# Optimization experiments

Hardware: AMD Instinct MI355X
Metric: run time of the kernel (lower is better)

## Reference

```python
import jax, jax.numpy as jnp
import numpy as np

N_NODES = 50000
N_EDGES = 800000
N_GRAPHS = 512
IN_DIM, HID_DIM, EMB_DIM = 128, 256, 128
EPS = 1e-5


def setup_inputs() -> dict:
    key = jax.random.key(0)
    ks = jax.random.split(key, 12)
    x = jax.random.normal(ks[0], (N_NODES, IN_DIM), dtype=jnp.float32)
    edge_index = jax.random.randint(ks[1], (2, N_EDGES), 0, N_NODES, dtype=jnp.int32)
    batch = jnp.sort(jax.random.randint(ks[2], (N_NODES,), 0, N_GRAPHS, dtype=jnp.int32))
    s1 = 1.0 / np.sqrt(IN_DIM)
    s2 = 1.0 / np.sqrt(HID_DIM)
    return {
        "x": x,
        "edge_index": edge_index,
        "batch": batch,
        "W1": jax.random.uniform(ks[3], (IN_DIM, HID_DIM), jnp.float32, -s1, s1),
        "b1": jnp.zeros((HID_DIM,), jnp.float32),
        "gamma1": jnp.ones((HID_DIM,), jnp.float32),
        "beta1": jnp.zeros((HID_DIM,), jnp.float32),
        "W2": jax.random.uniform(ks[4], (HID_DIM, EMB_DIM), jnp.float32, -s2, s2),
        "b2": jnp.zeros((EMB_DIM,), jnp.float32),
        "gamma2": jnp.ones((EMB_DIM,), jnp.float32),
        "beta2": jnp.zeros((EMB_DIM,), jnp.float32),
    }


def _gcn_conv(x, W, b, src, dst, n_nodes):
    # PyG GCNConv: h = xW; aggregate with sym-normalized adjacency incl. self-loops; + bias
    h = x @ W  # [N, D]
    ones = jnp.ones(src.shape[0], dtype=h.dtype)
    deg = jax.ops.segment_sum(ones, dst, num_segments=n_nodes) + 1.0  # self-loop
    dinv = jax.lax.rsqrt(deg)
    norm = dinv[src] * dinv[dst]  # [E]
    msg = h[src] * norm[:, None]  # gather + scale  [E, D]
    agg = jax.ops.segment_sum(msg, dst, num_segments=n_nodes)
    agg = agg + h * (1.0 / deg)[:, None]  # self-loop contribution (norm = 1/deg)
    return agg + b


def _batchnorm(h, gamma, beta):
    mean = jnp.mean(h, axis=0)
    var = jnp.mean(jnp.square(h - mean), axis=0)  # biased, training mode
    return gamma * (h - mean) * jax.lax.rsqrt(var + EPS) + beta


def reference(x, edge_index, batch, W1, b1, gamma1, beta1, W2, b2, gamma2, beta2):
    src, dst = edge_index[0], edge_index[1]
    n = x.shape[0]
    h = _gcn_conv(x, W1, b1, src, dst, n)
    h = _batchnorm(jax.nn.relu(h), gamma1, beta1)
    h = _gcn_conv(h, W2, b2, src, dst, n)
    h = _batchnorm(jax.nn.relu(h), gamma2, beta2)
    return jax.ops.segment_max(h, batch, num_segments=N_GRAPHS)
```

## Files before the change

kernel.cpp:

```cpp
#include <hip/hip_runtime.h>
#include <math.h>

#define N_NODES 50000
#define N_EDGES 800000
#define N_GRAPHS 512
#define IN_DIM 128
#define HID_DIM 256
#define EMB_DIM 128
#define EPS 1e-5f
#define ELLW 64
#define NGROUP 8
#define GROUPN 6250
#define BLK_PER_GROUP 256
#define EPB ((N_EDGES + BLK_PER_GROUP - 1) / BLK_PER_GROUP)
#define F2B_N (N_NODES * IN_DIM / 4)
#define F2B_BLOCKS ((F2B_N + 255) / 256)
#define TW1_BLOCKS ((HID_DIM * IN_DIM + 255) / 256)
#define DINV_BLOCKS ((N_NODES + 255) / 256)

typedef __attribute__((ext_vector_type(8))) short bf16x8;
typedef __attribute__((ext_vector_type(4))) float f32x4;

static __device__ __forceinline__ unsigned short f2b(float f) {
    unsigned u = __float_as_uint(f);
    return (unsigned short)((u + 0x7fffu + ((u >> 16) & 1u)) >> 16);
}
static __device__ __forceinline__ float b2f(unsigned short h) {
    return __uint_as_float(((unsigned)h) << 16);
}

__global__ void __launch_bounds__(256) scatter_xcd(const int* __restrict__ src,
                                                   const int* __restrict__ dst,
                                                   int* __restrict__ fill,
                                                   int* __restrict__ col) {
    int b = blockIdx.x;
    int g = b & 7;
    int bs = b >> 3;
    int lo = g * GROUPN;
    int hi = lo + GROUPN;
    int e_end = min((bs + 1) * EPB, N_EDGES);
    for (int e = bs * EPB + threadIdx.x; e < e_end; e += 256) {
        int d = dst[e];
        if (d >= lo && d < hi) {
            int pos = atomicAdd(&fill[d], 1);
            pos = min(pos, ELLW - 1);
            col[(d << 6) + pos] = src[e];
        }
    }
}

__global__ void convert_kernel(const float* __restrict__ x, unsigned short* __restrict__ xbf,
                               const float* __restrict__ W1, unsigned short* __restrict__ W1t,
                               const int* __restrict__ fill, float* __restrict__ dinv) {
    int b = blockIdx.x;
    if (b < F2B_BLOCKS) {
        int i = b * 256 + threadIdx.x;
        if (i < F2B_N) {
            float4 v = ((const float4*)x)[i];
            ushort4 o;
            o.x = f2b(v.x); o.y = f2b(v.y); o.z = f2b(v.z); o.w = f2b(v.w);
            ((ushort4*)xbf)[i] = o;
        }
    } else if (b < F2B_BLOCKS + TW1_BLOCKS) {
        int j = (b - F2B_BLOCKS) * 256 + threadIdx.x;
        if (j < HID_DIM * IN_DIM) {
            int n = j >> 7;
            int k = j & 127;
            W1t[j] = f2b(W1[k * HID_DIM + n]);
        }
    } else {
        int v = (b - F2B_BLOCKS - TW1_BLOCKS) * 256 + threadIdx.x;
        if (v < N_NODES) dinv[v] = rsqrtf((float)(min(fill[v], ELLW) + 1));
    }
}

static __device__ __forceinline__ void acc8(float* acc, uint4 r, float w) {
    const unsigned* u = (const unsigned*)&r;
#pragma unroll
    for (int k = 0; k < 4; ++k) {
        float lo = __uint_as_float((u[k] & 0xFFFFu) << 16);
        float hi = __uint_as_float(u[k] & 0xFFFF0000u);
        acc[2 * k]     += w * lo;
        acc[2 * k + 1] += w * hi;
    }
}

template <bool RELU, bool OUT_BF, bool BIAS>
__global__ void __launch_bounds__(256) aggw_kernel(const unsigned short* __restrict__ h,
                                                   const float* __restrict__ dinv,
                                                   const int* __restrict__ deg,
                                                   const int* __restrict__ col,
                                                   const float* __restrict__ bias,
                                                   void* __restrict__ y) {
    int tid = threadIdx.x;
    int lane = tid & 63;
    int wid = tid >> 6;
    int v = blockIdx.x * 4 + wid;
    int g = lane >> 4;
    int p = lane & 15;

    int beg = v << 6;
    int end = beg + min(deg[v], ELLW);
    float acc[8] = {};

    for (int e = beg; e < end; e += 16) {
        int i0 = e + g, i1 = e + 4 + g, i2 = e + 8 + g, i3 = e + 12 + g;
        int c0 = min(i0, end - 1), c1 = min(i1, end - 1);
        int c2 = min(i2, end - 1), c3 = min(i3, end - 1);
        int u0 = col[c0], u1 = col[c1], u2 = col[c2], u3 = col[c3];
        float w0 = (i0 < end) ? dinv[u0] : 0.f;
        float w1 = (i1 < end) ? dinv[u1] : 0.f;
        float w2 = (i2 < end) ? dinv[u2] : 0.f;
        float w3 = (i3 < end) ? dinv[u3] : 0.f;
        uint4 d0 = *(const uint4*)(h + (size_t)u0 * 128 + p * 8);
        uint4 d1 = *(const uint4*)(h + (size_t)u1 * 128 + p * 8);
        uint4 d2 = *(const uint4*)(h + (size_t)u2 * 128 + p * 8);
        uint4 d3 = *(const uint4*)(h + (size_t)u3 * 128 + p * 8);
        acc8(acc, d0, w0);
        acc8(acc, d1, w1);
        acc8(acc, d2, w2);
        acc8(acc, d3, w3);
    }

#pragma unroll
    for (int k = 0; k < 8; ++k) {
        float a = acc[k];
        a += __shfl_xor(a, 16, 64);
        a += __shfl_xor(a, 32, 64);
        acc[k] = a;
    }

    if (g == 0) {
        uint4 selfr = *(const uint4*)(h + (size_t)v * 128 + p * 8);
        const unsigned* su = (const unsigned*)&selfr;
        float dv = dinv[v];
        float dv2 = dv * dv;
        float o[8];
#pragma unroll
        for (int k = 0; k < 4; ++k) {
            float lo = __uint_as_float((su[k] & 0xFFFFu) << 16);
            float hi = __uint_as_float(su[k] & 0xFFFF0000u);
            o[2 * k]     = dv * acc[2 * k]     + lo * dv2;
            o[2 * k + 1] = dv * acc[2 * k + 1] + hi * dv2;
        }
        if (BIAS) {
            float4 bv0 = *(const float4*)&bias[p * 8];
            float4 bv1 = *(const float4*)&bias[p * 8 + 4];
            o[0] += bv0.x; o[1] += bv0.y; o[2] += bv0.z; o[3] += bv0.w;
            o[4] += bv1.x; o[5] += bv1.y; o[6] += bv1.z; o[7] += bv1.w;
        }
        if (RELU) {
#pragma unroll
            for (int k = 0; k < 8; ++k) o[k] = fmaxf(o[k], 0.f);
        }
        if (OUT_BF) {
            uint4 packed;
            unsigned* pu = (unsigned*)&packed;
#pragma unroll
            for (int k = 0; k < 4; ++k)
                pu[k] = (unsigned)f2b(o[2 * k]) | ((unsigned)f2b(o[2 * k + 1]) << 16);
            *(uint4*)((unsigned short*)y + (size_t)v * 128 + p * 8) = packed;
        } else {
            float* yf = (float*)y + (size_t)v * 128 + p * 8;
            *(float4*)yf = make_float4(o[0], o[1], o[2], o[3]);
            *(float4*)(yf + 4) = make_float4(o[4], o[5], o[6], o[7]);
        }
    }
}

template <bool RELU>
__global__ void __launch_bounds__(256) mfma_gemm_kernel(const unsigned short* __restrict__ A,
                                                        const unsigned short* __restrict__ Bt,
                                                        const float* __restrict__ bias,
                                                        unsigned short* __restrict__ C,
                                                        int M, int N, int K) {
    const int LDT = 40;
    __shared__ unsigned short As[64 * LDT];
    __shared__ unsigned short Bs[64 * LDT];
    int tid = threadIdx.x;
    int bm = blockIdx.x * 64;
    int bn = blockIdx.y * 64;
    int lr = tid >> 2;
    int lc = (tid & 3) * 8;
    int lane = tid & 63;
    int w = tid >> 6;
    int wr = (w >> 1) * 32, wc = (w & 1) * 32;
    int l15 = lane & 15, q = lane >> 4;

    f32x4 acc[2][2] = {};
    bool arow_ok = (bm + lr) < M;
    const unsigned short* Aptr = A + (size_t)(bm + lr) * K + lc;
    const unsigned short* Bptr = Bt + (size_t)(bn + lr) * K + lc;

    for (int k0 = 0; k0 < K; k0 += 32) {
        uint4 av = arow_ok ? *(const uint4*)(Aptr + k0) : make_uint4(0u, 0u, 0u, 0u);
        uint4 bv = *(const uint4*)(Bptr + k0);
        *(uint4*)&As[lr * LDT + lc] = av;
        *(uint4*)&Bs[lr * LDT + lc] = bv;
        __syncthreads();
        bf16x8 a0 = *(const bf16x8*)&As[(wr + 0 + l15) * LDT + q * 8];
        bf16x8 a1 = *(const bf16x8*)&As[(wr + 16 + l15) * LDT + q * 8];
        bf16x8 b0 = *(const bf16x8*)&Bs[(wc + 0 + l15) * LDT + q * 8];
        bf16x8 b1 = *(const bf16x8*)&Bs[(wc + 16 + l15) * LDT + q * 8];
        acc[0][0] = __builtin_amdgcn_mfma_f32_16x16x32_bf16(a0, b0, acc[0][0], 0, 0, 0);
        acc[0][1] = __builtin_amdgcn_mfma_f32_16x16x32_bf16(a0, b1, acc[0][1], 0, 0, 0);
        acc[1][0] = __builtin_amdgcn_mfma_f32_16x16x32_bf16(a1, b0, acc[1][0], 0, 0, 0);
        acc[1][1] = __builtin_amdgcn_mfma_f32_16x16x32_bf16(a1, b1, acc[1][1], 0, 0, 0);
        __syncthreads();
    }

#pragma unroll
    for (int mi = 0; mi < 2; ++mi)
#pragma unroll
        for (int ni = 0; ni < 2; ++ni) {
            int colc = bn + wc + ni * 16 + l15;
            float bv = bias ? bias[colc] : 0.f;
#pragma unroll
            for (int r = 0; r < 4; ++r) {
                int row = bm + wr + mi * 16 + q * 4 + r;
                if (row < M) {
                    float vv = acc[mi][ni][r] + bv;
                    if (RELU) vv = fmaxf(vv, 0.f);
                    C[(size_t)row * N + colc] = f2b(vv);
                }
            }
        }
}

template <int C, bool BF>
__global__ void __launch_bounds__(256) stats_fast(const void* __restrict__ yv,
                                                  float* __restrict__ sum,
                                                  float* __restrict__ sumsq) {
    constexpr int VEC = BF ? 8 : 4;
    constexpr int NCHUNK = C / VEC;
    constexpr int ROWS = 256 / NCHUNK;
    constexpr int STRIDE = 256 * ROWS;
    __shared__ float sp[256 * VEC];
    __shared__ float qp[256 * VEC];
    int t = threadIdx.x;
    int j = t & (NCHUNK - 1);
    float s[VEC], q[VEC];
#pragma unroll
    for (int k = 0; k < VEC; ++k) { s[k] = 0.f; q[k] = 0.f; }

    const char* base = (const char*)yv + (size_t)j * 16;
    auto body = [&](int v) {
        uint4 raw = *(const uint4*)(base + (size_t)v * (C * (BF ? 2 : 4)));
        float x[VEC];
        if (BF) {
            const unsigned* u = (const unsigned*)&raw;
#pragma unroll
            for (int k = 0; k < 4; ++k) {
                x[2 * k]     = __uint_as_float((u[k] & 0xFFFFu) << 16);
                x[2 * k + 1] = __uint_as_float(u[k] & 0xFFFF0000u);
            }
        } else {
            const float* f = (const float*)&raw;
#pragma unroll
            for (int k = 0; k < VEC; ++k) x[k] = f[k];
        }
#pragma unroll
        for (int k = 0; k < VEC; ++k) { s[k] += x[k]; q[k] += x[k] * x[k]; }
    };

    int v = blockIdx.x * ROWS + (t >> 5);
    for (; v + 3 * STRIDE < N_NODES; v += 4 * STRIDE) {
        body(v); body(v + STRIDE); body(v + 2 * STRIDE); body(v + 3 * STRIDE);
    }
    for (; v < N_NODES; v += STRIDE) body(v);

#pragma unroll
    for (int k = 0; k < VEC; ++k) { sp[t * VEC + k] = s[k]; qp[t * VEC + k] = q[k]; }
    __syncthreads();
    if (t < C) {
        float ss = 0.f, qq = 0.f;
#pragma unroll
        for (int rr = 0; rr < ROWS; ++rr) {
            ss += sp[rr * (NCHUNK * VEC) + t];
            qq += qp[rr * (NCHUNK * VEC) + t];
        }
        atomicAdd(&sum[t], ss);
        atomicAdd(&sumsq[t], qq);
    }
}

__global__ void prep2_kernel(const float* __restrict__ sum1, const float* __restrict__ sumsq1,
                             const float* __restrict__ gamma1, const float* __restrict__ beta1,
                             const float* __restrict__ W2, unsigned short* __restrict__ W2pt,
                             float* __restrict__ bc2) {
    __shared__ float a1s[HID_DIM], s1s[HID_DIM];
    int t = threadIdx.x;
    {
        float m = sum1[t] * (1.f / N_NODES);
        float var = sumsq1[t] * (1.f / N_NODES) - m * m;
        float a = gamma1[t] * rsqrtf(var + EPS);
        a1s[t] = a;
        s1s[t] = beta1[t] - m * a;
    }
    __syncthreads();
    if (t < EMB_DIM) {
        float bacc = 0.f;
        for (int k = 0; k < HID_DIM; ++k) {
            float w = W2[k * EMB_DIM + t];
            W2pt[t * HID_DIM + k] = f2b(a1s[k] * w);
            bacc += s1s[k] * w;
        }
        bc2[t] = bacc;
    }
}

__global__ void __launch_bounds__(128) segmax_kernel(const float* __restrict__ y,
                                                     const float* __restrict__ sum2,
                                                     const float* __restrict__ sumsq2,
                                                     const float* __restrict__ gamma2,
                                                     const float* __restrict__ beta2,
                                                     const int* __restrict__ batch,
                                                     float* __restrict__ out) {
    __shared__ int sh[2];
    int g = blockIdx.x;
    int c = threadIdx.x;
    float mch = sum2[c] * (1.f / N_NODES);
    float var = sumsq2[c] * (1.f / N_NODES) - mch * mch;
    float ac = gamma2[c] * rsqrtf(var + EPS);
    float sc = beta2[c] - mch * ac;
    if (threadIdx.x == 0) {
        int lo = 0, hi = N_NODES;
        while (lo < hi) { int mid = (lo + hi) >> 1; if (batch[mid] < g) lo = mid + 1; else hi = mid; }
        sh[0] = lo;
        hi = N_NODES;
        while (lo < hi) { int mid = (lo + hi) >> 1; if (batch[mid] < g + 1) lo = mid + 1; else hi = mid; }
        sh[1] = lo;
    }
    __syncthreads();
    int beg = sh[0], end = sh[1];
    float m = -INFINITY;
    for (int v = beg; v < end; ++v) {
        m = fmaxf(m, fmaf(ac, y[(size_t)v * EMB_DIM + c], sc));
    }
    out[(size_t)g * EMB_DIM + c] = m;
}

extern "C" void kernel_launch(void* const* d_in, const int* in_sizes, int n_in,
                              void* d_out, int out_size, void* d_ws, size_t ws_size,
                              hipStream_t stream) {
    const float* x      = (const float*)d_in[0];
    const int*   ei     = (const int*)d_in[1];
    const int*   batch  = (const int*)d_in[2];
    const float* W1     = (const float*)d_in[3];
    const float* b1     = (const float*)d_in[4];
    const float* gamma1 = (const float*)d_in[5];
    const float* beta1  = (const float*)d_in[6];
    const float* W2     = (const float*)d_in[7];
    const float* b2     = (const float*)d_in[8];
    const float* gamma2 = (const float*)d_in[9];
    const float* beta2  = (const float*)d_in[10];
    float* out = (float*)d_out;

    char* ws = (char*)d_ws;
    size_t off = 0;
    auto alloc = [&](size_t bytes) -> char* {
        char* p = ws + off;
        off = (off + bytes + 255) & ~(size_t)255;
        return p;
    };
    int*   fill   = (int*)alloc((size_t)N_NODES * 4);
    float* stats  = (float*)alloc(1024 * 4);
    size_t zbytes = off;
    int*   col    = (int*)alloc((size_t)N_NODES * ELLW * 4);
    float* dinv   = (float*)alloc((size_t)N_NODES * 4);
    float* bc2    = (float*)alloc((size_t)EMB_DIM * 4);
    unsigned short* W1t  = (unsigned short*)alloc((size_t)HID_DIM * IN_DIM * 2);
    unsigned short* W2pt = (unsigned short*)alloc((size_t)HID_DIM * EMB_DIM * 2);
    unsigned short* xbf  = (unsigned short*)alloc((size_t)N_NODES * IN_DIM * 2);
    unsigned short* axbf = (unsigned short*)alloc((size_t)N_NODES * IN_DIM * 2);
    unsigned short* y1bf = (unsigned short*)alloc((size_t)N_NODES * HID_DIM * 2);
    unsigned short* gbf  = (unsigned short*)alloc((size_t)N_NODES * EMB_DIM * 2);
    float* y2 = (float*)xbf;
    (void)ws_size; (void)in_sizes; (void)n_in; (void)out_size;

    const int* src  = ei;
    const int* dstp = ei + N_EDGES;

    hipMemsetAsync(ws, 0, zbytes, stream);

    scatter_xcd<<<NGROUP * BLK_PER_GROUP, 256, 0, stream>>>(src, dstp, fill, col);
    convert_kernel<<<F2B_BLOCKS + TW1_BLOCKS + DINV_BLOCKS, 256, 0, stream>>>(
        x, xbf, W1, W1t, fill, dinv);

    aggw_kernel<false, true, false><<<N_NODES / 4, 256, 0, stream>>>(xbf, dinv, fill, col, nullptr, axbf);
    dim3 g1((N_NODES + 63) / 64, HID_DIM / 64);
    mfma_gemm_kernel<true><<<g1, 256, 0, stream>>>(axbf, W1t, b1, y1bf, N_NODES, HID_DIM, IN_DIM);
    stats_fast<HID_DIM, true><<<256, 256, 0, stream>>>(y1bf, stats, stats + 256);

    prep2_kernel<<<1, 256, 0, stream>>>(stats, stats + 256, gamma1, beta1, W2, W2pt, bc2);

    dim3 g2((N_NODES + 63) / 64, EMB_DIM / 64);
    mfma_gemm_kernel<false><<<g2, 256, 0, stream>>>(y1bf, W2pt, bc2, gbf,
                                                    N_NODES, EMB_DIM, HID_DIM);
    aggw_kernel<true, false, true><<<N_NODES / 4, 256, 0, stream>>>(gbf, dinv, fill, col, b2, y2);
    stats_fast<EMB_DIM, false><<<256, 256, 0, stream>>>(y2, stats + 512, stats + 640);

    segmax_kernel<<<N_GRAPHS, 128, 0, stream>>>(y2, stats + 512, stats + 640,
                                                gamma2, beta2, batch, out);
}
```

Before: 303.0 us.

## Merge scatter and convert kernels, compute dinv inline, store layer-2 output as bf16

Folds the edge scatter, x/W1 conversion into a single launch and drops the separate dinv array by recomputing rsqrt from the fill counts inside the aggregation kernels. The second aggregation now writes bf16 instead of fp32, and stats and segmax read bf16. This removes one launch and halves the traffic of the final activations, at the cost of extra precision loss in the second-layer output and an added rsqrt per gathered neighbour.

```diff
diff --git a/kernel.cpp b/kernel.cpp
--- a/kernel.cpp
+++ b/kernel.cpp
@@ -12,11 +12,11 @@
 #define NGROUP 8
 #define GROUPN 6250
 #define BLK_PER_GROUP 256
+#define SCAT_BLOCKS (NGROUP * BLK_PER_GROUP)
 #define EPB ((N_EDGES + BLK_PER_GROUP - 1) / BLK_PER_GROUP)
 #define F2B_N (N_NODES * IN_DIM / 4)
 #define F2B_BLOCKS ((F2B_N + 255) / 256)
 #define TW1_BLOCKS ((HID_DIM * IN_DIM + 255) / 256)
-#define DINV_BLOCKS ((N_NODES + 255) / 256)
 
 typedef __attribute__((ext_vector_type(8))) short bf16x8;
 typedef __attribute__((ext_vector_type(4))) float f32x4;
@@ -28,49 +28,48 @@
 static __device__ __forceinline__ float b2f(unsigned short h) {
     return __uint_as_float(((unsigned)h) << 16);
 }
-
-__global__ void __launch_bounds__(256) scatter_xcd(const int* __restrict__ src,
-                                                   const int* __restrict__ dst,
-                                                   int* __restrict__ fill,
-                                                   int* __restrict__ col) {
+static __device__ __forceinline__ float deg2w(int d) {
+    return rsqrtf((float)(min(d, ELLW) + 1));
+}
+
+__global__ void __launch_bounds__(256) build_kernel(const int* __restrict__ src,
+                                                    const int* __restrict__ dst,
+                                                    int* __restrict__ fill,
+                                                    int* __restrict__ col,
+                                                    const float* __restrict__ x,
+                                                    unsigned short* __restrict__ xbf,
+                                                    const float* __restrict__ W1,
+                                                    unsigned short* __restrict__ W1t) {
     int b = blockIdx.x;
-    int g = b & 7;
-    int bs = b >> 3;
-    int lo = g * GROUPN;
-    int hi = lo + GROUPN;
-    int e_end = min((bs + 1) * EPB, N_EDGES);
-    for (int e = bs * EPB + threadIdx.x; e < e_end; e += 256) {
-        int d = dst[e];
-        if (d >= lo && d < hi) {
-            int pos = atomicAdd(&fill[d], 1);
-            pos = min(pos, ELLW - 1);
-            col[(d << 6) + pos] = src[e];
-        }
-    }
-}
-
-__global__ void convert_kernel(const float* __restrict__ x, unsigned short* __restrict__ xbf,
-                               const float* __restrict__ W1, unsigned short* __restrict__ W1t,
-                               const int* __restrict__ fill, float* __restrict__ dinv) {
-    int b = blockIdx.x;
-    if (b < F2B_BLOCKS) {
-        int i = b * 256 + threadIdx.x;
+    if (b < SCAT_BLOCKS) {
+        int g = b & 7;
+        int bs = b >> 3;
+        int lo = g * GROUPN;
+        int hi = lo + GROUPN;
+        int e_end = min((bs + 1) * EPB, N_EDGES);
+        for (int e = bs * EPB + threadIdx.x; e < e_end; e += 256) {
+            int d = dst[e];
+            if (d >= lo && d < hi) {
+                int pos = atomicAdd(&fill[d], 1);
+                pos = min(pos, ELLW - 1);
+                col[(d << 6) + pos] = src[e];
+            }
+        }
+    } else if (b < SCAT_BLOCKS + F2B_BLOCKS) {
+        int i = (b - SCAT_BLOCKS) * 256 + threadIdx.x;
         if (i < F2B_N) {
             float4 v = ((const float4*)x)[i];
             ushort4 o;
             o.x = f2b(v.x); o.y = f2b(v.y); o.z = f2b(v.z); o.w = f2b(v.w);
             ((ushort4*)xbf)[i] = o;
         }
-    } else if (b < F2B_BLOCKS + TW1_BLOCKS) {
-        int j = (b - F2B_BLOCKS) * 256 + threadIdx.x;
+    } else {
+        int j = (b - SCAT_BLOCKS - F2B_BLOCKS) * 256 + threadIdx.x;
         if (j < HID_DIM * IN_DIM) {
             int n = j >> 7;
             int k = j & 127;
             W1t[j] = f2b(W1[k * HID_DIM + n]);
         }
-    } else {
-        int v = (b - F2B_BLOCKS - TW1_BLOCKS) * 256 + threadIdx.x;
-        if (v < N_NODES) dinv[v] = rsqrtf((float)(min(fill[v], ELLW) + 1));
     }
 }
 
@@ -85,13 +84,12 @@
     }
 }
 
-template <bool RELU, bool OUT_BF, bool BIAS>
+template <bool RELU, bool BIAS>
 __global__ void __launch_bounds__(256) aggw_kernel(const unsigned short* __restrict__ h,
-                                                   const float* __restrict__ dinv,
                                                    const int* __restrict__ deg,
                                                    const int* __restrict__ col,
                                                    const float* __restrict__ bias,
-                                                   void* __restrict__ y) {
+                                                   unsigned short* __restrict__ y) {
     int tid = threadIdx.x;
     int lane = tid & 63;
     int wid = tid >> 6;
@@ -108,10 +106,10 @@
         int c0 = min(i0, end - 1), c1 = min(i1, end - 1);
         int c2 = min(i2, end - 1), c3 = min(i3, end - 1);
         int u0 = col[c0], u1 = col[c1], u2 = col[c2], u3 = col[c3];
-        float w0 = (i0 < end) ? dinv[u0] : 0.f;
-        float w1 = (i1 < end) ? dinv[u1] : 0.f;
-        float w2 = (i2 < end) ? dinv[u2] : 0.f;
-        float w3 = (i3 < end) ? dinv[u3] : 0.f;
+        float w0 = (i0 < end) ? deg2w(deg[u0]) : 0.f;
+        float w1 = (i1 < end) ? deg2w(deg[u1]) : 0.f;
+        float w2 = (i2 < end) ? deg2w(deg[u2]) : 0.f;
+        float w3 = (i3 < end) ? deg2w(deg[u3]) : 0.f;
         uint4 d0 = *(const uint4*)(h + (size_t)u0 * 128 + p * 8);
         uint4 d1 = *(const uint4*)(h + (size_t)u1 * 128 + p * 8);
         uint4 d2 = *(const uint4*)(h + (size_t)u2 * 128 + p * 8);
@@ -133,7 +131,7 @@
     if (g == 0) {
         uint4 selfr = *(const uint4*)(h + (size_t)v * 128 + p * 8);
         const unsigned* su = (const unsigned*)&selfr;
-        float dv = dinv[v];
+        float dv = deg2w(deg[v]);
         float dv2 = dv * dv;
         float o[8];
 #pragma unroll
@@ -153,18 +151,12 @@
 #pragma unroll
             for (int k = 0; k < 8; ++k) o[k] = fmaxf(o[k], 0.f);
         }
-        if (OUT_BF) {
-            uint4 packed;
-            unsigned* pu = (unsigned*)&packed;
-#pragma unroll
-            for (int k = 0; k < 4; ++k)
-                pu[k] = (unsigned)f2b(o[2 * k]) | ((unsigned)f2b(o[2 * k + 1]) << 16);
-            *(uint4*)((unsigned short*)y + (size_t)v * 128 + p * 8) = packed;
-        } else {
-            float* yf = (float*)y + (size_t)v * 128 + p * 8;
-            *(float4*)yf = make_float4(o[0], o[1], o[2], o[3]);
-            *(float4*)(yf + 4) = make_float4(o[4], o[5], o[6], o[7]);
-        }
+        uint4 packed;
+        unsigned* pu = (unsigned*)&packed;
+#pragma unroll
+        for (int k = 0; k < 4; ++k)
+            pu[k] = (unsigned)f2b(o[2 * k]) | ((unsigned)f2b(o[2 * k + 1]) << 16);
+        *(uint4*)(y + (size_t)v * 128 + p * 8) = packed;
     }
 }
 
@@ -227,11 +219,11 @@
         }
 }
 
-template <int C, bool BF>
-__global__ void __launch_bounds__(256) stats_fast(const void* __restrict__ yv,
+template <int C>
+__global__ void __launch_bounds__(256) stats_fast(const unsigned short* __restrict__ yv,
                                                   float* __restrict__ sum,
                                                   float* __restrict__ sumsq) {
-    constexpr int VEC = BF ? 8 : 4;
+    constexpr int VEC = 8;
     constexpr int NCHUNK = C / VEC;
     constexpr int ROWS = 256 / NCHUNK;
     constexpr int STRIDE = 256 * ROWS;
@@ -243,27 +235,21 @@
 #pragma unroll
     for (int k = 0; k < VEC; ++k) { s[k] = 0.f; q[k] = 0.f; }
 
-    const char* base = (const char*)yv + (size_t)j * 16;
+    const unsigned short* base = yv + (size_t)j * 8;
     auto body = [&](int v) {
-        uint4 raw = *(const uint4*)(base + (size_t)v * (C * (BF ? 2 : 4)));
+        uint4 raw = *(const uint4*)(base + (size_t)v * C);
+        const unsigned* u = (const unsigned*)&raw;
         float x[VEC];
-        if (BF) {
-            const unsigned* u = (const unsigned*)&raw;
-#pragma unroll
-            for (int k = 0; k < 4; ++k) {
-                x[2 * k]     = __uint_as_float((u[k] & 0xFFFFu) << 16);
-                x[2 * k + 1] = __uint_as_float(u[k] & 0xFFFF0000u);
-            }
-        } else {
-            const float* f = (const float*)&raw;
-#pragma unroll
-            for (int k = 0; k < VEC; ++k) x[k] = f[k];
+#pragma unroll
+        for (int k = 0; k < 4; ++k) {
+            x[2 * k]     = __uint_as_float((u[k] & 0xFFFFu) << 16);
+            x[2 * k + 1] = __uint_as_float(u[k] & 0xFFFF0000u);
         }
 #pragma unroll
         for (int k = 0; k < VEC; ++k) { s[k] += x[k]; q[k] += x[k] * x[k]; }
     };
 
-    int v = blockIdx.x * ROWS + (t >> 5);
+    int v = blockIdx.x * ROWS + (t / NCHUNK);
     for (; v + 3 * STRIDE < N_NODES; v += 4 * STRIDE) {
         body(v); body(v + STRIDE); body(v + 2 * STRIDE); body(v + 3 * STRIDE);
     }
@@ -309,7 +295,7 @@
     }
 }
 
-__global__ void __launch_bounds__(128) segmax_kernel(const float* __restrict__ y,
+__global__ void __launch_bounds__(128) segmax_kernel(const unsigned short* __restrict__ y,
                                                      const float* __restrict__ sum2,
                                                      const float* __restrict__ sumsq2,
                                                      const float* __restrict__ gamma2,
@@ -335,7 +321,7 @@
     int beg = sh[0], end = sh[1];
     float m = -INFINITY;
     for (int v = beg; v < end; ++v) {
-        m = fmaxf(m, fmaf(ac, y[(size_t)v * EMB_DIM + c], sc));
+        m = fmaxf(m, fmaf(ac, b2f(y[(size_t)v * EMB_DIM + c]), sc));
     }
     out[(size_t)g * EMB_DIM + c] = m;
 }
@@ -367,7 +353,6 @@
     float* stats  = (float*)alloc(1024 * 4);
     size_t zbytes = off;
     int*   col    = (int*)alloc((size_t)N_NODES * ELLW * 4);
-    float* dinv   = (float*)alloc((size_t)N_NODES * 4);
     float* bc2    = (float*)alloc((size_t)EMB_DIM * 4);
     unsigned short* W1t  = (unsigned short*)alloc((size_t)HID_DIM * IN_DIM * 2);
     unsigned short* W2pt = (unsigned short*)alloc((size_t)HID_DIM * EMB_DIM * 2);
@@ -375,7 +360,7 @@
     unsigned short* axbf = (unsigned short*)alloc((size_t)N_NODES * IN_DIM * 2);
     unsigned short* y1bf = (unsigned short*)alloc((size_t)N_NODES * HID_DIM * 2);
     unsigned short* gbf  = (unsigned short*)alloc((size_t)N_NODES * EMB_DIM * 2);
-    float* y2 = (float*)xbf;
+    unsigned short* y2 = xbf;
     (void)ws_size; (void)in_sizes; (void)n_in; (void)out_size;
 
     const int* src  = ei;
@@ -383,22 +368,21 @@
 
     hipMemsetAsync(ws, 0, zbytes, stream);
 
-    scatter_xcd<<<NGROUP * BLK_PER_GROUP, 256, 0, stream>>>(src, dstp, fill, col);
-    convert_kernel<<<F2B_BLOCKS + TW1_BLOCKS + DINV_BLOCKS, 256, 0, stream>>>(
-        x, xbf, W1, W1t, fill, dinv);
-
-    aggw_kernel<false, true, false><<<N_NODES / 4, 256, 0, stream>>>(xbf, dinv, fill, col, nullptr, axbf);
+    build_kernel<<<SCAT_BLOCKS + F2B_BLOCKS + TW1_BLOCKS, 256, 0, stream>>>(
+        src, dstp, fill, col, x, xbf, W1, W1t);
+
+    aggw_kernel<false, false><<<N_NODES / 4, 256, 0, stream>>>(xbf, fill, col, nullptr, axbf);
     dim3 g1((N_NODES + 63) / 64, HID_DIM / 64);
     mfma_gemm_kernel<true><<<g1, 256, 0, stream>>>(axbf, W1t, b1, y1bf, N_NODES, HID_DIM, IN_DIM);
-    stats_fast<HID_DIM, true><<<256, 256, 0, stream>>>(y1bf, stats, stats + 256);
+    stats_fast<HID_DIM><<<256, 256, 0, stream>>>(y1bf, stats, stats + 256);
 
     prep2_kernel<<<1, 256, 0, stream>>>(stats, stats + 256, gamma1, beta1, W2, W2pt, bc2);
 
     dim3 g2((N_NODES + 63) / 64, EMB_DIM / 64);
     mfma_gemm_kernel<false><<<g2, 256, 0, stream>>>(y1bf, W2pt, bc2, gbf,
                                                     N_NODES, EMB_DIM, HID_DIM);
-    aggw_kernel<true, false, true><<<N_NODES / 4, 256, 0, stream>>>(gbf, dinv, fill, col, b2, y2);
-    stats_fast<EMB_DIM, false><<<256, 256, 0, stream>>>(y2, stats + 512, stats + 640);
+    aggw_kernel<true, true><<<N_NODES / 4, 256, 0, stream>>>(gbf, fill, col, b2, y2);
+    stats_fast<EMB_DIM><<<256, 256, 0, stream>>>(y2, stats + 512, stats + 640);
 
     segmax_kernel<<<N_GRAPHS, 128, 0, stream>>>(y2, stats + 512, stats + 640,
                                                 gamma2, beta2, batch, out);
```

New measurement: 305.3 us. About the same (+0.7%).
